# Kernel optimization log

Hardware: AMD Instinct MI355X
Metric: run time of the kernel (lower is better)

The kernel has to match this reference:

```python
import jax, jax.numpy as jnp
import numpy as np

H, DH, CHUNK = 8, 64, 64      # heads, dim_head, chunk_size
DIM = 512
INNER = H * DH                # 512
EPS = 1e-5
SCALE = DH ** -0.5


def _ln(x, g, b):
    m = jnp.mean(x, -1, keepdims=True)
    v = jnp.mean((x - m) ** 2, -1, keepdims=True)
    return (x - m) * jax.lax.rsqrt(v + EPS) * g + b


def _heads(t):
    b, n, _ = t.shape
    return t.reshape(b, n, H, DH).transpose(0, 2, 1, 3)  # b h n d


def _merge(t):
    b, h, n, d = t.shape
    return t.transpose(0, 2, 1, 3).reshape(b, n, h * d)  # b n (h d)


def _local_attn(x, W_qkv, W_ao, b_ao):
    # PreNorm inner Attention: non-overlapping chunked local self-attention
    qkv = x @ W_qkv
    q, k, v = (jnp.split(qkv, 3, axis=-1))
    q, k, v = _heads(q), _heads(k), _heads(v)
    B, Hh, N, D = q.shape
    M = N // CHUNK
    qc = q.reshape(B, Hh, M, CHUNK, D)
    kc = k.reshape(B, Hh, M, CHUNK, D)
    vc = v.reshape(B, Hh, M, CHUNK, D)
    s = jnp.einsum('bhmcd,bhmkd->bhmck', qc, kc) * SCALE
    a = jax.nn.softmax(s, axis=-1)
    o = jnp.einsum('bhmck,bhmkd->bhmcd', a, vc).reshape(B, Hh, N, D)
    return _merge(o) @ W_ao + b_ao


def setup_inputs() -> dict:
    key = jax.random.key(0)
    ks = jax.random.split(key, 10)
    p = lambda k, shp: jax.random.normal(k, shp, dtype=jnp.float32) * 0.02
    return {
        'x':     jax.random.normal(ks[0], (2, 4096, DIM), dtype=jnp.float32),
        'q_x':   jax.random.normal(ks[1], (2, 2048, DIM), dtype=jnp.float32),
        'ln1_g': jnp.ones((DIM,), jnp.float32),
        'ln1_b': jnp.zeros((DIM,), jnp.float32),
        'W_qkv': p(ks[2], (DIM, INNER * 3)),
        'W_ao':  p(ks[3], (INNER, DIM)),
        'b_ao':  jnp.zeros((DIM,), jnp.float32),
        'ln2_g': jnp.ones((DIM,), jnp.float32),
        'ln2_b': jnp.zeros((DIM,), jnp.float32),
        'W_q':   p(ks[4], (DIM, INNER)),
        'W_kv':  p(ks[5], (DIM, INNER * 2)),
        'W_o':   p(ks[6], (INNER, DIM)),
        'b_o':   jnp.zeros((DIM,), jnp.float32),
    }


def reference(x, q_x, ln1_g, ln1_b, W_qkv, W_ao, b_ao,
              ln2_g, ln2_b, W_q, W_kv, W_o, b_o):
    # inner chunked self-attn with PreNorm + residual
    q_in = _local_attn(_ln(q_x, ln1_g, ln1_b), W_qkv, W_ao, b_ao) + q_x
    q_in = _ln(q_in, ln2_g, ln2_b)
    # full cross-attention: queries from q_in, keys/values from x
    q = _heads(q_in @ W_q)
    k, v = jnp.split(x @ W_kv, 2, axis=-1)
    k, v = _heads(k), _heads(v)
    s = jnp.einsum('bhqd,bhkd->bhqk', q, k) * SCALE
    a = jax.nn.softmax(s, axis=-1)
    out = _merge(jnp.einsum('bhqk,bhkd->bhqd', a, v)) @ W_o + b_o
    return (out, q_in)
```

## Files before the change

kernel.cpp:

```cpp
#include <hip/hip_runtime.h>

typedef unsigned short u16;
typedef unsigned int u32;
typedef __attribute__((ext_vector_type(4))) float f32x4;
typedef __attribute__((ext_vector_type(8))) __bf16 bf16x8;

#define NQ 2048
#define NK 4096
#define SCALE 0.125f
#define LOG2E 1.44269504088896f

__device__ __forceinline__ u16 f2bf(float f) {
  u32 x = __float_as_uint(f);
  return (u16)((x + 0x7fffu + ((x >> 16) & 1u)) >> 16);
}

__device__ __forceinline__ float bf2f(u16 b) {
  return __uint_as_float(((u32)b) << 16);
}

__device__ __forceinline__ int swz(int row, int colbyte) {
  return row * 128 + (colbyte ^ ((row & 7) << 4));
}

__device__ __forceinline__ void async16(u16* lds, const u16* g) {
  __builtin_amdgcn_global_load_lds(
      (const __attribute__((address_space(1))) void*)g,
      (__attribute__((address_space(3))) void*)lds, 16, 0, 0);
}

__device__ __forceinline__ f32x4 mfma16(bf16x8 a, bf16x8 b, f32x4 c) {
  return __builtin_amdgcn_mfma_f32_16x16x32_bf16(a, b, c, 0, 0, 0);
}

__device__ __forceinline__ float max16(const f32x4* s) {
  float a = fmaxf(fmaxf(s[0][0], s[0][1]), fmaxf(s[0][2], s[0][3]));
  float b = fmaxf(fmaxf(s[1][0], s[1][1]), fmaxf(s[1][2], s[1][3]));
  float c = fmaxf(fmaxf(s[2][0], s[2][1]), fmaxf(s[2][2], s[2][3]));
  float d = fmaxf(fmaxf(s[3][0], s[3][1]), fmaxf(s[3][2], s[3][3]));
  return fmaxf(fmaxf(a, b), fmaxf(c, d));
}

__global__ __launch_bounds__(256) void k_prep(
    const float* __restrict__ Wqkv, const float* __restrict__ Wao,
    const float* __restrict__ Wq, const float* __restrict__ Wkv,
    const float* __restrict__ Wo, const float* __restrict__ x,
    const float* __restrict__ qx, const float* __restrict__ ln1g,
    const float* __restrict__ ln1b,
    u16* __restrict__ o_qkv, u16* __restrict__ o_ao, u16* __restrict__ o_q,
    u16* __restrict__ o_kv, u16* __restrict__ o_o, u16* __restrict__ x_bf,
    u16* __restrict__ xn_bf) {
  int bid = blockIdx.x;
  int t = threadIdx.x;
  if (bid < 8192) {
    int idx = bid * 256 + t;
    int r = idx >> 9, k = idx & 511;
    const float* in;
    u16* out;
    int N, n;
    if (r < 1536)      { in = Wqkv; out = o_qkv; N = 1536; n = r; }
    else if (r < 2048) { in = Wao;  out = o_ao;  N = 512;  n = r - 1536; }
    else if (r < 2560) { in = Wq;   out = o_q;   N = 512;  n = r - 2048; }
    else if (r < 3584) { in = Wkv;  out = o_kv;  N = 1024; n = r - 2560; }
    else               { in = Wo;   out = o_o;   N = 512;  n = r - 3584; }
    out[(size_t)n * 512 + k] = f2bf(in[(size_t)k * N + n]);
  } else if (bid < 10240) {
    size_t i = ((size_t)(bid - 8192) * 256 + t) * 8;
    float v[8];
    *(float4*)&v[0] = *(const float4*)(x + i);
    *(float4*)&v[4] = *(const float4*)(x + i + 4);
    u16 o[8];
#pragma unroll
    for (int j = 0; j < 8; j++) o[j] = f2bf(v[j]);
    *(uint4*)(x_bf + i) = *(uint4*)o;
  } else {
    int row = (bid - 10240) * 4 + (t >> 6);
    int lane = t & 63;
    size_t base = (size_t)row * 512 + lane * 8;
    float v[8];
    *(float4*)&v[0] = *(const float4*)(qx + base);
    *(float4*)&v[4] = *(const float4*)(qx + base + 4);
    float s = 0.f, q = 0.f;
#pragma unroll
    for (int j = 0; j < 8; j++) { s += v[j]; q += v[j] * v[j]; }
#pragma unroll
    for (int d = 1; d < 64; d <<= 1) {
      s += __shfl_xor(s, d, 64);
      q += __shfl_xor(q, d, 64);
    }
    float mean = s * (1.f / 512.f);
    float var = q * (1.f / 512.f) - mean * mean;
    float rstd = rsqrtf(var + 1e-5f);
    float gv[8], bv[8];
    *(float4*)&gv[0] = *(const float4*)(ln1g + lane * 8);
    *(float4*)&gv[4] = *(const float4*)(ln1g + lane * 8 + 4);
    *(float4*)&bv[0] = *(const float4*)(ln1b + lane * 8);
    *(float4*)&bv[4] = *(const float4*)(ln1b + lane * 8 + 4);
    u16 ob[8];
#pragma unroll
    for (int j = 0; j < 8; j++)
      ob[j] = f2bf((v[j] - mean) * rstd * gv[j] + bv[j]);
    *(uint4*)(xn_bf + base) = *(uint4*)ob;
  }
}

__global__ __launch_bounds__(64) void k_ln(const float* __restrict__ xin,
                                           const float* __restrict__ res,
                                           const float* __restrict__ gg,
                                           const float* __restrict__ bb,
                                           float* __restrict__ fout,
                                           u16* __restrict__ bfout) {
  int row = blockIdx.x, t = threadIdx.x;
  size_t base = (size_t)row * 512 + t * 8;
  float v[8];
  *(float4*)&v[0] = *(const float4*)(xin + base);
  *(float4*)&v[4] = *(const float4*)(xin + base + 4);
  if (res) {
    float r2[8];
    *(float4*)&r2[0] = *(const float4*)(res + base);
    *(float4*)&r2[4] = *(const float4*)(res + base + 4);
#pragma unroll
    for (int j = 0; j < 8; j++) v[j] += r2[j];
  }
  float s = 0.f, q = 0.f;
#pragma unroll
  for (int j = 0; j < 8; j++) { s += v[j]; q += v[j] * v[j]; }
#pragma unroll
  for (int d = 1; d < 64; d <<= 1) {
    s += __shfl_xor(s, d, 64);
    q += __shfl_xor(q, d, 64);
  }
  float mean = s * (1.f / 512.f);
  float var = q * (1.f / 512.f) - mean * mean;
  float rstd = rsqrtf(var + 1e-5f);
  float gv[8], bv[8];
  *(float4*)&gv[0] = *(const float4*)(gg + t * 8);
  *(float4*)&gv[4] = *(const float4*)(gg + t * 8 + 4);
  *(float4*)&bv[0] = *(const float4*)(bb + t * 8);
  *(float4*)&bv[4] = *(const float4*)(bb + t * 8 + 4);
  float y[8];
  u16 ob[8];
#pragma unroll
  for (int j = 0; j < 8; j++) {
    y[j] = (v[j] - mean) * rstd * gv[j] + bv[j];
    ob[j] = f2bf(y[j]);
  }
  if (fout) {
    *(float4*)(fout + base) = *(float4*)&y[0];
    *(float4*)(fout + base + 4) = *(float4*)&y[4];
  }
  if (bfout) *(uint4*)(bfout + base) = *(uint4*)ob;
}

__global__ __launch_bounds__(256) void k_mm0(
    const u16* __restrict__ xb, const u16* __restrict__ wkv,
    const u16* __restrict__ xn, const u16* __restrict__ wqkv,
    u16* __restrict__ kpk, u16* __restrict__ vtp, u16* __restrict__ qkv) {
  __shared__ u16 As[8192];
  __shared__ u16 Bs[8192];
  const int tid = threadIdx.x;
  const int lane = tid & 63, wid = tid >> 6;
  const int lr = lane & 15, g = lane >> 4;
  const int wr = wid >> 1, wc = wid & 1;
  const int srow = wid * 8 + (lane >> 3);
  const int scol = ((lane & 7) ^ (lane >> 3)) << 3;
  u16* lA = As + wid * 512;
  u16* lB = Bs + wid * 512;
  const size_t rK = (size_t)32 * 512;
  int bid = blockIdx.x;
  if (bid < 512) {
    int bx = bid & 7, by = bid >> 3;
    const int rowBase = by * 128, colBase = bx * 128;
    f32x4 acc[4][4] = {};
    const u16* gA = xb + (size_t)(rowBase + srow) * 512 + scol;
    const u16* gB = wkv + (size_t)(colBase + srow) * 512 + scol;
    for (int k0 = 0; k0 < 512; k0 += 64) {
#pragma unroll
      for (int r = 0; r < 4; r++) async16(lA + r * 2048, gA + r * rK + k0);
#pragma unroll
      for (int r = 0; r < 4; r++) async16(lB + r * 2048, gB + r * rK + k0);
      __syncthreads();
#pragma unroll
      for (int kk = 0; kk < 2; kk++) {
        bf16x8 af[4], bw[4];
#pragma unroll
        for (int fm = 0; fm < 4; fm++) {
          int row = wr * 64 + fm * 16 + lr;
          af[fm] = *(const bf16x8*)((const char*)As + row * 128 +
                                    (((kk * 4 + g) ^ (row & 7)) << 4));
        }
#pragma unroll
        for (int fn = 0; fn < 4; fn++) {
          int row = wc * 64 + fn * 16 + lr;
          bw[fn] = *(const bf16x8*)((const char*)Bs + row * 128 +
                                    (((kk * 4 + g) ^ (row & 7)) << 4));
        }
#pragma unroll
        for (int fm = 0; fm < 4; fm++)
#pragma unroll
          for (int fn = 0; fn < 4; fn++)
            acc[fm][fn] = mfma16(af[fm], bw[fn], acc[fm][fn]);
      }
      __syncthreads();
    }
#pragma unroll
    for (int fm = 0; fm < 4; fm++) {
#pragma unroll
      for (int fn = 0; fn < 4; fn++) {
        int row = rowBase + wr * 64 + fm * 16 + g * 4;
        int col = colBase + wc * 64 + fn * 16 + lr;
        int b = row >> 12, n = row & 4095, kt = n >> 6, key0 = n & 63;
        int h = (col >> 6) & 7, d = col & 63;
        size_t tbase = ((size_t)(((b << 3) + h) << 6) + kt) * 4096;
        if (col < 512) {
          u16* kd = kpk + tbase + (size_t)key0 * 64 + d;
          kd[0] = f2bf(acc[fm][fn][0]);
          kd[64] = f2bf(acc[fm][fn][1]);
          kd[128] = f2bf(acc[fm][fn][2]);
          kd[192] = f2bf(acc[fm][fn][3]);
        } else {
          u16 p4[4] = {f2bf(acc[fm][fn][0]), f2bf(acc[fm][fn][1]),
                       f2bf(acc[fm][fn][2]), f2bf(acc[fm][fn][3])};
          *(uint2*)(vtp + tbase + (size_t)d * 64 + key0) = *(uint2*)p4;
        }
      }
    }
  } else {
    int j = bid - 512;
    int bx = j % 12, by = j / 12;
    const int rowBase = by * 64, colBase = bx * 128;
    f32x4 acc[2][4] = {};
    const u16* gA = xn + (size_t)(rowBase + srow) * 512 + scol;
    const u16* gB = wqkv + (size_t)(colBase + srow) * 512 + scol;
    for (int k0 = 0; k0 < 512; k0 += 64) {
#pragma unroll
      for (int r = 0; r < 2; r++) async16(lA + r * 2048, gA + r * rK + k0);
#pragma unroll
      for (int r = 0; r < 4; r++) async16(lB + r * 2048, gB + r * rK + k0);
      __syncthreads();
#pragma unroll
      for (int kk = 0; kk < 2; kk++) {
        bf16x8 af[2], bw[4];
#pragma unroll
        for (int fm = 0; fm < 2; fm++) {
          int row = wr * 32 + fm * 16 + lr;
          af[fm] = *(const bf16x8*)((const char*)As + row * 128 +
                                    (((kk * 4 + g) ^ (row & 7)) << 4));
        }
#pragma unroll
        for (int fn = 0; fn < 4; fn++) {
          int row = wc * 64 + fn * 16 + lr;
          bw[fn] = *(const bf16x8*)((const char*)Bs + row * 128 +
                                    (((kk * 4 + g) ^ (row & 7)) << 4));
        }
#pragma unroll
        for (int fm = 0; fm < 2; fm++)
#pragma unroll
          for (int fn = 0; fn < 4; fn++)
            acc[fm][fn] = mfma16(af[fm], bw[fn], acc[fm][fn]);
      }
      __syncthreads();
    }
#pragma unroll
    for (int fm = 0; fm < 2; fm++) {
#pragma unroll
      for (int fn = 0; fn < 4; fn++) {
        int row = rowBase + wr * 32 + fm * 16 + g * 4;
        int col = colBase + wc * 64 + fn * 16 + lr;
#pragma unroll
        for (int r = 0; r < 4; r++)
          qkv[(size_t)(row + r) * 1536 + col] = f2bf(acc[fm][fn][r]);
      }
    }
  }
}

template <bool BIAS, bool OBF16>
__global__ __launch_bounds__(256) void k_gemm3(const u16* __restrict__ A,
                                               const u16* __restrict__ Bt,
                                               const float* __restrict__ bias,
                                               void* __restrict__ C, int M, int N, int K) {
  __shared__ u16 As[4096];
  __shared__ u16 Bs[4096];
  const int tid = threadIdx.x;
  const int lane = tid & 63, wid = tid >> 6;
  const int lr = lane & 15, g = lane >> 4;
  const int wr = wid >> 1, wc = wid & 1;
  const int rowBase = blockIdx.y * 64, colBase = blockIdx.x * 64;
  f32x4 acc[2][2] = {};
  const int srow = wid * 8 + (lane >> 3);
  const int scol = ((lane & 7) ^ (lane >> 3)) << 3;
  const u16* gA = A + (size_t)(rowBase + srow) * K + scol;
  const u16* gB = Bt + (size_t)(colBase + srow) * K + scol;
  u16* lA = As + wid * 512;
  u16* lB = Bs + wid * 512;
  const size_t rK = (size_t)32 * K;
  for (int k0 = 0; k0 < K; k0 += 64) {
#pragma unroll
    for (int r = 0; r < 2; r++) async16(lA + r * 2048, gA + r * rK + k0);
#pragma unroll
    for (int r = 0; r < 2; r++) async16(lB + r * 2048, gB + r * rK + k0);
    __syncthreads();
#pragma unroll
    for (int kk = 0; kk < 2; kk++) {
      bf16x8 af[2], bw[2];
#pragma unroll
      for (int fm = 0; fm < 2; fm++) {
        int row = wr * 32 + fm * 16 + lr;
        af[fm] = *(const bf16x8*)((const char*)As + row * 128 +
                                  (((kk * 4 + g) ^ (row & 7)) << 4));
      }
#pragma unroll
      for (int fn = 0; fn < 2; fn++) {
        int row = wc * 32 + fn * 16 + lr;
        bw[fn] = *(const bf16x8*)((const char*)Bs + row * 128 +
                                  (((kk * 4 + g) ^ (row & 7)) << 4));
      }
#pragma unroll
      for (int fm = 0; fm < 2; fm++)
#pragma unroll
        for (int fn = 0; fn < 2; fn++)
          acc[fm][fn] = mfma16(af[fm], bw[fn], acc[fm][fn]);
    }
    __syncthreads();
  }
#pragma unroll
  for (int fm = 0; fm < 2; fm++) {
#pragma unroll
    for (int fn = 0; fn < 2; fn++) {
      int row = rowBase + wr * 32 + fm * 16 + g * 4;
      int col = colBase + wc * 32 + fn * 16 + lr;
      float bvv = BIAS ? bias[col] : 0.f;
#pragma unroll
      for (int r = 0; r < 4; r++) {
        float v = acc[fm][fn][r] + bvv;
        if (OBF16)
          ((u16*)C)[(size_t)(row + r) * N + col] = f2bf(v);
        else
          ((float*)C)[(size_t)(row + r) * N + col] = v;
      }
    }
  }
}

__global__ __launch_bounds__(256) void k_local(const u16* __restrict__ qkv,
                                               u16* __restrict__ oattn) {
  int bid = blockIdx.x;
  int m = bid & 31, h = (bid >> 5) & 7, b = bid >> 8;
  __shared__ u16 Qs[4096], Ks[4096], Vt[4096], Ps[4096];
  int t = threadIdx.x;
  {
    int i = t >> 2, c0 = (t & 3) * 16;
    const u16* base = qkv + (size_t)(b * NQ + m * 64 + i) * 1536 + c0;
    uint4 q0 = *(const uint4*)(base + h * 64);
    uint4 q1 = *(const uint4*)(base + h * 64 + 8);
    uint4 k0 = *(const uint4*)(base + 512 + h * 64);
    uint4 k1 = *(const uint4*)(base + 512 + h * 64 + 8);
    uint4 v0 = *(const uint4*)(base + 1024 + h * 64);
    uint4 v1 = *(const uint4*)(base + 1024 + h * 64 + 8);
    *(uint4*)((char*)Qs + swz(i, c0 * 2)) = q0;
    *(uint4*)((char*)Qs + swz(i, c0 * 2 + 16)) = q1;
    *(uint4*)((char*)Ks + swz(i, c0 * 2)) = k0;
    *(uint4*)((char*)Ks + swz(i, c0 * 2 + 16)) = k1;
    u16 vv[16];
    *(uint4*)&vv[0] = v0;
    *(uint4*)&vv[8] = v1;
#pragma unroll
    for (int j = 0; j < 16; j++) {
      int d = c0 + j;
      *(u16*)((char*)Vt + swz(d, i * 2)) = vv[j];
    }
  }
  __syncthreads();
  int lane = t & 63, w = t >> 6, lr = lane & 15, g = lane >> 4;
  bf16x8 aq[2];
#pragma unroll
  for (int kk = 0; kk < 2; kk++)
    aq[kk] = *(const bf16x8*)((const char*)Qs + swz(w * 16 + lr, kk * 64 + g * 16));
  f32x4 s[4] = {};
#pragma unroll
  for (int fn = 0; fn < 4; fn++)
#pragma unroll
    for (int kk = 0; kk < 2; kk++) {
      bf16x8 bk = *(const bf16x8*)((const char*)Ks + swz(fn * 16 + lr, kk * 64 + g * 16));
      s[fn] = mfma16(aq[kk], bk, s[fn]);
    }
  float mx[4], sm[4], p[4][4];
#pragma unroll
  for (int r = 0; r < 4; r++)
    mx[r] = fmaxf(fmaxf(s[0][r], s[1][r]), fmaxf(s[2][r], s[3][r]));
#pragma unroll
  for (int d = 1; d < 16; d <<= 1)
#pragma unroll
    for (int r = 0; r < 4; r++) mx[r] = fmaxf(mx[r], __shfl_xor(mx[r], d, 64));
#pragma unroll
  for (int r = 0; r < 4; r++) {
    float a = 0.f;
#pragma unroll
    for (int fn = 0; fn < 4; fn++) {
      p[fn][r] = exp2f((s[fn][r] - mx[r]) * (SCALE * LOG2E));
      a += p[fn][r];
    }
    sm[r] = a;
  }
#pragma unroll
  for (int d = 1; d < 16; d <<= 1)
#pragma unroll
    for (int r = 0; r < 4; r++) sm[r] += __shfl_xor(sm[r], d, 64);
  float rinv[4];
#pragma unroll
  for (int r = 0; r < 4; r++) rinv[r] = 1.f / sm[r];
#pragma unroll
  for (int fn = 0; fn < 4; fn++)
#pragma unroll
    for (int r = 0; r < 4; r++)
      *(u16*)((char*)Ps + swz(w * 16 + g * 4 + r, (fn * 16 + lr) * 2)) =
          f2bf(p[fn][r] * rinv[r]);
  bf16x8 ap[2];
#pragma unroll
  for (int kk = 0; kk < 2; kk++)
    ap[kk] = *(const bf16x8*)((const char*)Ps + swz(w * 16 + lr, kk * 64 + g * 16));
  f32x4 o[4] = {};
#pragma unroll
  for (int fn = 0; fn < 4; fn++)
#pragma unroll
    for (int kk = 0; kk < 2; kk++) {
      bf16x8 bv = *(const bf16x8*)((const char*)Vt + swz(fn * 16 + lr, kk * 64 + g * 16));
      o[fn] = mfma16(ap[kk], bv, o[fn]);
    }
#pragma unroll
  for (int fn = 0; fn < 4; fn++)
#pragma unroll
    for (int r = 0; r < 4; r++)
      oattn[(size_t)(b * NQ + m * 64 + w * 16 + g * 4 + r) * 512 + h * 64 + fn * 16 + lr] =
          f2bf(o[fn][r]);
}

__global__ __launch_bounds__(256, 4) void k_cross(const u16* __restrict__ q,
                                                  const u16* __restrict__ kpk,
                                                  const u16* __restrict__ vtp,
                                                  u16* __restrict__ opart,
                                                  float* __restrict__ ml) {
  int f = blockIdx.x + 16 * blockIdx.y + 256 * blockIdx.z;
  int xcd = f & 7, j = f >> 3;
  int c = xcd + 8 * (j >> 4);
  int qt = j & 15, bh = c & 15, split = c >> 4;
  int b = bh >> 3, h = bh & 7;
  int t = threadIdx.x, lane = t & 63, w = t >> 6, lr = lane & 15, g = lane >> 4;
  __shared__ u16 Ks[2][4096], Vs[2][4096];
  const float cs = SCALE * LOG2E;

  bf16x8 ones;
#pragma unroll
  for (int i = 0; i < 8; i++) ones[i] = (__bf16)1.0f;

  int srow = w * 16 + (lane >> 3);
  int scolb = ((lane & 7) ^ (srow & 7)) << 3;
  int kperm = ((srow >> 5) << 5) + (((srow >> 2) & 3) << 3) +
              (((srow >> 4) & 1) << 2) + (srow & 3);
  int ksoff0 = kperm * 64 + scolb;
  int ksoff1 = ksoff0 + 1024;
  int soff0 = srow * 64 + scolb;
  int soff1 = soff0 + 512;
  const u16* ktiles = kpk + ((size_t)(bh * 64 + split * 16) * 4096);
  const u16* vtiles = vtp + ((size_t)(bh * 64 + split * 16) * 4096);

  const u16* qrowL = q + (size_t)(b * NQ + qt * 128 + w * 32 + lr) * 512 + h * 64;
  const u16* qrowH = qrowL + 16 * 512;
  bf16x8 aqL0 = *(const bf16x8*)(qrowL + g * 8);
  bf16x8 aqL1 = *(const bf16x8*)(qrowL + 32 + g * 8);
  bf16x8 aqH0 = *(const bf16x8*)(qrowH + g * 8);
  bf16x8 aqH1 = *(const bf16x8*)(qrowH + 32 + g * 8);

  f32x4 oL[4] = {}, oH[4] = {};
  f32x4 lsumL = {}, lsumH = {};
  float mL = -1e30f, mH = -1e30f;

  async16(&Ks[0][w * 1024], ktiles + ksoff0);
  async16(&Ks[0][w * 1024 + 512], ktiles + ksoff1);
  async16(&Vs[0][w * 1024], vtiles + soff0);
  async16(&Vs[0][w * 1024 + 512], vtiles + soff1);
  __syncthreads();

  int buf = 0;
  for (int kt = 0; kt < 16; kt++) {
    if (kt < 15) {
      const u16* kn = ktiles + (size_t)(kt + 1) * 4096;
      const u16* vn = vtiles + (size_t)(kt + 1) * 4096;
      async16(&Ks[buf ^ 1][w * 1024], kn + ksoff0);
      async16(&Ks[buf ^ 1][w * 1024 + 512], kn + ksoff1);
      async16(&Vs[buf ^ 1][w * 1024], vn + soff0);
      async16(&Vs[buf ^ 1][w * 1024 + 512], vn + soff1);
    }
    f32x4 stL[4], stH[4];
    __builtin_amdgcn_s_setprio(1);
#pragma unroll
    for (int fm = 0; fm < 4; fm++) {
      bf16x8 bk0 = *(const bf16x8*)((const char*)Ks[buf] + swz(fm * 16 + lr, g * 16));
      bf16x8 bk1 = *(const bf16x8*)((const char*)Ks[buf] + swz(fm * 16 + lr, 64 + g * 16));
      stL[fm] = mfma16(bk0, aqL0, (f32x4){0.f, 0.f, 0.f, 0.f});
      stL[fm] = mfma16(bk1, aqL1, stL[fm]);
      stH[fm] = mfma16(bk0, aqH0, (f32x4){0.f, 0.f, 0.f, 0.f});
      stH[fm] = mfma16(bk1, aqH1, stH[fm]);
    }
    __builtin_amdgcn_s_setprio(0);
    float tmL = max16(stL);
    tmL = fmaxf(tmL, __shfl_xor(tmL, 16, 64));
    tmL = fmaxf(tmL, __shfl_xor(tmL, 32, 64));
    if (!__all(tmL <= mL + 22.2f)) {
      float mnew = fmaxf(mL, tmL);
      float corr = exp2f((mL - mnew) * cs);
      mL = mnew;
      float c0 = __shfl(corr, g * 4 + 0, 64);
      float c1 = __shfl(corr, g * 4 + 1, 64);
      float c2 = __shfl(corr, g * 4 + 2, 64);
      float c3 = __shfl(corr, g * 4 + 3, 64);
      lsumL[0] *= c0; lsumL[1] *= c1; lsumL[2] *= c2; lsumL[3] *= c3;
#pragma unroll
      for (int fn = 0; fn < 4; fn++) {
        oL[fn][0] *= c0; oL[fn][1] *= c1; oL[fn][2] *= c2; oL[fn][3] *= c3;
      }
    }
    bf16x8 apL0, apL1;
    {
      float mc = mL * cs;
      union { __bf16 hh[8]; bf16x8 v; } u0, u1;
#pragma unroll
      for (int r = 0; r < 4; r++) {
        u0.hh[r]     = (__bf16)exp2f(stL[0][r] * cs - mc);
        u0.hh[4 + r] = (__bf16)exp2f(stL[1][r] * cs - mc);
        u1.hh[r]     = (__bf16)exp2f(stL[2][r] * cs - mc);
        u1.hh[4 + r] = (__bf16)exp2f(stL[3][r] * cs - mc);
      }
      apL0 = u0.v;
      apL1 = u1.v;
    }
    float tmH = max16(stH);
    tmH = fmaxf(tmH, __shfl_xor(tmH, 16, 64));
    tmH = fmaxf(tmH, __shfl_xor(tmH, 32, 64));
    if (!__all(tmH <= mH + 22.2f)) {
      float mnew = fmaxf(mH, tmH);
      float corr = exp2f((mH - mnew) * cs);
      mH = mnew;
      float c0 = __shfl(corr, g * 4 + 0, 64);
      float c1 = __shfl(corr, g * 4 + 1, 64);
      float c2 = __shfl(corr, g * 4 + 2, 64);
      float c3 = __shfl(corr, g * 4 + 3, 64);
      lsumH[0] *= c0; lsumH[1] *= c1; lsumH[2] *= c2; lsumH[3] *= c3;
#pragma unroll
      for (int fn = 0; fn < 4; fn++) {
        oH[fn][0] *= c0; oH[fn][1] *= c1; oH[fn][2] *= c2; oH[fn][3] *= c3;
      }
    }
    bf16x8 apH0, apH1;
    {
      float mc = mH * cs;
      union { __bf16 hh[8]; bf16x8 v; } u0, u1;
#pragma unroll
      for (int r = 0; r < 4; r++) {
        u0.hh[r]     = (__bf16)exp2f(stH[0][r] * cs - mc);
        u0.hh[4 + r] = (__bf16)exp2f(stH[1][r] * cs - mc);
        u1.hh[r]     = (__bf16)exp2f(stH[2][r] * cs - mc);
        u1.hh[4 + r] = (__bf16)exp2f(stH[3][r] * cs - mc);
      }
      apH0 = u0.v;
      apH1 = u1.v;
    }
    __builtin_amdgcn_s_setprio(1);
    lsumL = mfma16(apL0, ones, lsumL);
    lsumL = mfma16(apL1, ones, lsumL);
    lsumH = mfma16(apH0, ones, lsumH);
    lsumH = mfma16(apH1, ones, lsumH);
#pragma unroll
    for (int fn = 0; fn < 4; fn++) {
      bf16x8 bv0 = *(const bf16x8*)((const char*)Vs[buf] + swz(fn * 16 + lr, g * 16));
      bf16x8 bv1 = *(const bf16x8*)((const char*)Vs[buf] + swz(fn * 16 + lr, 64 + g * 16));
      oL[fn] = mfma16(apL0, bv0, oL[fn]);
      oL[fn] = mfma16(apL1, bv1, oL[fn]);
      oH[fn] = mfma16(apH0, bv0, oH[fn]);
      oH[fn] = mfma16(apH1, bv1, oH[fn]);
    }
    __builtin_amdgcn_s_setprio(0);
    __syncthreads();
    buf ^= 1;
  }
  size_t sb = ((size_t)(split * 16 + bh) * NQ) + qt * 128 + w * 32;
  {
    float r0 = 1.f / lsumL[0], r1 = 1.f / lsumL[1];
    float r2 = 1.f / lsumL[2], r3 = 1.f / lsumL[3];
#pragma unroll
    for (int fn = 0; fn < 4; fn++) {
      opart[(sb + g * 4 + 0) * 64 + fn * 16 + lr] = f2bf(oL[fn][0] * r0);
      opart[(sb + g * 4 + 1) * 64 + fn * 16 + lr] = f2bf(oL[fn][1] * r1);
      opart[(sb + g * 4 + 2) * 64 + fn * 16 + lr] = f2bf(oL[fn][2] * r2);
      opart[(sb + g * 4 + 3) * 64 + fn * 16 + lr] = f2bf(oL[fn][3] * r3);
    }
  }
  {
    float r0 = 1.f / lsumH[0], r1 = 1.f / lsumH[1];
    float r2 = 1.f / lsumH[2], r3 = 1.f / lsumH[3];
#pragma unroll
    for (int fn = 0; fn < 4; fn++) {
      opart[(sb + 16 + g * 4 + 0) * 64 + fn * 16 + lr] = f2bf(oH[fn][0] * r0);
      opart[(sb + 16 + g * 4 + 1) * 64 + fn * 16 + lr] = f2bf(oH[fn][1] * r1);
      opart[(sb + 16 + g * 4 + 2) * 64 + fn * 16 + lr] = f2bf(oH[fn][2] * r2);
      opart[(sb + 16 + g * 4 + 3) * 64 + fn * 16 + lr] = f2bf(oH[fn][3] * r3);
    }
  }
  if (g == 0) {
    ml[(sb + lr) * 2] = mL;
    ml[(sb + 16 + lr) * 2] = mH;
  }
  if (lr == 0) {
#pragma unroll
    for (int r = 0; r < 4; r++) {
      ml[(sb + g * 4 + r) * 2 + 1] = lsumL[r];
      ml[(sb + 16 + g * 4 + r) * 2 + 1] = lsumH[r];
    }
  }
}

__global__ __launch_bounds__(256) void k_comb(const u16* __restrict__ opart,
                                              const float* __restrict__ ml,
                                              u16* __restrict__ co) {
  int idx = blockIdx.x * 256 + threadIdx.x;
  int c8 = idx & 7;
  int row = (idx >> 3) & 2047;
  int bh = idx >> 14;
  int b = bh >> 3, h = bh & 7;
  const float cs = SCALE * LOG2E;
  float m[4], l[4];
#pragma unroll
  for (int s = 0; s < 4; s++) {
    size_t rb = ((size_t)(s * 16 + bh) * NQ + row);
    m[s] = ml[rb * 2];
    l[s] = ml[rb * 2 + 1];
  }
  float M = fmaxf(fmaxf(m[0], m[1]), fmaxf(m[2], m[3]));
  float wsum = 0.f, wgt[4];
#pragma unroll
  for (int s = 0; s < 4; s++) {
    wgt[s] = l[s] * exp2f((m[s] - M) * cs);
    wsum += wgt[s];
  }
  float acc[8] = {};
#pragma unroll
  for (int s = 0; s < 4; s++) {
    size_t rb = ((size_t)(s * 16 + bh) * NQ + row);
    uint4 pk = *(const uint4*)(opart + rb * 64 + c8 * 8);
    u16 pe[8];
    *(uint4*)pe = pk;
#pragma unroll
    for (int j = 0; j < 8; j++) acc[j] += wgt[s] * bf2f(pe[j]);
  }
  float rw = 1.f / wsum;
  u16 ob[8];
#pragma unroll
  for (int j = 0; j < 8; j++) ob[j] = f2bf(acc[j] * rw);
  *(uint4*)(co + ((size_t)(b * NQ + row) * 512) + h * 64 + c8 * 8) = *(uint4*)ob;
}

extern "C" void kernel_launch(void* const* d_in, const int* in_sizes, int n_in,
                              void* d_out, int out_size, void* d_ws, size_t ws_size,
                              hipStream_t stream) {
  const float* x    = (const float*)d_in[0];
  const float* qx   = (const float*)d_in[1];
  const float* ln1g = (const float*)d_in[2];
  const float* ln1b = (const float*)d_in[3];
  const float* Wqkv = (const float*)d_in[4];
  const float* Wao  = (const float*)d_in[5];
  const float* bao  = (const float*)d_in[6];
  const float* ln2g = (const float*)d_in[7];
  const float* ln2b = (const float*)d_in[8];
  const float* Wq   = (const float*)d_in[9];
  const float* Wkv  = (const float*)d_in[10];
  const float* Wo   = (const float*)d_in[11];
  const float* bo   = (const float*)d_in[12];
  float* out_p = (float*)d_out;
  float* qin_p = out_p + (size_t)2 * 2048 * 512;

  const size_t MiB = 1048576;
  char* ws = (char*)d_ws;
  u16* w_qkv_t = (u16*)(ws);
  u16* w_ao_t  = (u16*)(ws + 1572864);
  u16* w_q_t   = (u16*)(ws + 2097152);
  u16* w_kv_t  = (u16*)(ws + 2621440);
  u16* w_o_t   = (u16*)(ws + 3670016);
  u16* kpk     = (u16*)(ws + 4 * MiB);
  u16* vtp     = (u16*)(ws + 12 * MiB);
  u16* x_bf    = (u16*)(ws + 20 * MiB);
  u16* oattn_bf = (u16*)(ws + 20 * MiB);
  float* ao_f  = (float*)(ws + 24 * MiB);
  u16* xn_bf   = (u16*)(ws + 28 * MiB);
  u16* qin_bf  = (u16*)(ws + 32 * MiB);
  u16* opart   = (u16*)(ws + 20 * MiB);
  u16* qkv_bf  = (u16*)(ws + 36 * MiB);
  u16* q_bf    = (u16*)(ws + 36 * MiB);
  u16* co_bf   = (u16*)(ws + 40 * MiB);
  float* ml    = out_p;

  k_prep<<<dim3(8192 + 2048 + 1024), 256, 0, stream>>>(
      Wqkv, Wao, Wq, Wkv, Wo, x, qx, ln1g, ln1b,
      w_qkv_t, w_ao_t, w_q_t, w_kv_t, w_o_t, x_bf, xn_bf);
  k_mm0<<<dim3(512 + 768), 256, 0, stream>>>(
      x_bf, w_kv_t, xn_bf, w_qkv_t, kpk, vtp, qkv_bf);
  k_local<<<dim3(512), 256, 0, stream>>>(qkv_bf, oattn_bf);
  k_gemm3<true, false><<<dim3(512 / 64, 4096 / 64), 256, 0, stream>>>(
      oattn_bf, w_ao_t, bao, ao_f, 4096, 512, 512);
  k_ln<<<dim3(4096), 64, 0, stream>>>(ao_f, qx, ln2g, ln2b, qin_p, qin_bf);
  k_gemm3<false, true><<<dim3(512 / 64, 4096 / 64), 256, 0, stream>>>(
      qin_bf, w_q_t, nullptr, q_bf, 4096, 512, 512);
  k_cross<<<dim3(16, 16, 4), 256, 0, stream>>>(q_bf, kpk, vtp, opart, ml);
  k_comb<<<dim3(262144 / 256), 256, 0, stream>>>(opart, ml, co_bf);
  k_gemm3<true, false><<<dim3(512 / 64, 4096 / 64), 256, 0, stream>>>(
      co_bf, w_o_t, bo, out_p, 4096, 512, 512);
}
```

Baseline: 153.8 us.

## Fuse split-KV combine into output projection GEMM and store ao in bf16

```diff
diff --git a/kernel.cpp b/kernel.cpp
--- a/kernel.cpp
+++ b/kernel.cpp
@@ -104,7 +104,7 @@
   }
 }
 
-__global__ __launch_bounds__(64) void k_ln(const float* __restrict__ xin,
+__global__ __launch_bounds__(64) void k_ln(const u16* __restrict__ xin,
                                            const float* __restrict__ res,
                                            const float* __restrict__ gg,
                                            const float* __restrict__ bb,
@@ -112,10 +112,12 @@
                                            u16* __restrict__ bfout) {
   int row = blockIdx.x, t = threadIdx.x;
   size_t base = (size_t)row * 512 + t * 8;
+  u16 xv[8];
+  *(uint4*)xv = *(const uint4*)(xin + base);
   float v[8];
-  *(float4*)&v[0] = *(const float4*)(xin + base);
-  *(float4*)&v[4] = *(const float4*)(xin + base + 4);
-  if (res) {
+#pragma unroll
+  for (int j = 0; j < 8; j++) v[j] = bf2f(xv[j]);
+  {
     float r2[8];
     *(float4*)&r2[0] = *(const float4*)(res + base);
     *(float4*)&r2[4] = *(const float4*)(res + base + 4);
@@ -145,11 +147,9 @@
     y[j] = (v[j] - mean) * rstd * gv[j] + bv[j];
     ob[j] = f2bf(y[j]);
   }
-  if (fout) {
-    *(float4*)(fout + base) = *(float4*)&y[0];
-    *(float4*)(fout + base + 4) = *(float4*)&y[4];
-  }
-  if (bfout) *(uint4*)(bfout + base) = *(uint4*)ob;
+  *(float4*)(fout + base) = *(float4*)&y[0];
+  *(float4*)(fout + base + 4) = *(float4*)&y[4];
+  *(uint4*)(bfout + base) = *(uint4*)ob;
 }
 
 __global__ __launch_bounds__(256) void k_mm0(
@@ -343,6 +343,105 @@
   }
 }
 
+__global__ __launch_bounds__(256) void k_gout(const u16* __restrict__ opart,
+                                              const float* __restrict__ ml,
+                                              const u16* __restrict__ wo_t,
+                                              const float* __restrict__ bias,
+                                              float* __restrict__ C) {
+  __shared__ u16 As[4096];
+  __shared__ u16 Bs[4096];
+  const int tid = threadIdx.x;
+  const int lane = tid & 63, wid = tid >> 6;
+  const int lr = lane & 15, g = lane >> 4;
+  const int wr = wid >> 1, wc = wid & 1;
+  const int rowBase = blockIdx.y * 64, colBase = blockIdx.x * 64;
+  f32x4 acc[2][2] = {};
+  const int srow = wid * 8 + (lane >> 3);
+  const int slot = lane & 7;
+  const int scolB = ((lane & 7) ^ (lane >> 3)) << 3;
+  const u16* gB = wo_t + (size_t)(colBase + srow) * 512 + scolB;
+  u16* lB = Bs + wid * 512;
+  const size_t rK = (size_t)32 * 512;
+  const float cs = SCALE * LOG2E;
+  for (int k0 = 0; k0 < 512; k0 += 64) {
+#pragma unroll
+    for (int r = 0; r < 2; r++) async16(lB + r * 2048, gB + r * rK + k0);
+    int h = k0 >> 6;
+#pragma unroll
+    for (int r = 0; r < 2; r++) {
+      int lrow = srow + r * 32;
+      int row = rowBase + lrow;
+      int b = row >> 11, nq = row & 2047;
+      int bh = (b << 3) + h;
+      size_t rr[4];
+      float mm[4], ll[4];
+#pragma unroll
+      for (int s = 0; s < 4; s++) {
+        rr[s] = ((size_t)(s * 16 + bh) * 2048 + nq);
+        mm[s] = ml[rr[s] * 2];
+        ll[s] = ml[rr[s] * 2 + 1];
+      }
+      float M = fmaxf(fmaxf(mm[0], mm[1]), fmaxf(mm[2], mm[3]));
+      float wn[4], wsum = 0.f;
+#pragma unroll
+      for (int s = 0; s < 4; s++) {
+        wn[s] = ll[s] * exp2f((mm[s] - M) * cs);
+        wsum += wn[s];
+      }
+      float rw = 1.f / wsum;
+#pragma unroll
+      for (int s = 0; s < 4; s++) wn[s] *= rw;
+      float a8[8] = {};
+#pragma unroll
+      for (int s = 0; s < 4; s++) {
+        u16 pe[8];
+        *(uint4*)pe = *(const uint4*)(opart + rr[s] * 64 + slot * 8);
+#pragma unroll
+        for (int j = 0; j < 8; j++) a8[j] += wn[s] * bf2f(pe[j]);
+      }
+      u16 o8[8];
+#pragma unroll
+      for (int j = 0; j < 8; j++) o8[j] = f2bf(a8[j]);
+      *(uint4*)((char*)As + lrow * 128 + ((slot ^ (lrow & 7)) << 4)) = *(uint4*)o8;
+    }
+    __syncthreads();
+#pragma unroll
+    for (int kk = 0; kk < 2; kk++) {
+      bf16x8 af[2], bw[2];
+#pragma unroll
+      for (int fm = 0; fm < 2; fm++) {
+        int row = wr * 32 + fm * 16 + lr;
+        af[fm] = *(const bf16x8*)((const char*)As + row * 128 +
+                                  (((kk * 4 + g) ^ (row & 7)) << 4));
+      }
+#pragma unroll
+      for (int fn = 0; fn < 2; fn++) {
+        int row = wc * 32 + fn * 16 + lr;
+        bw[fn] = *(const bf16x8*)((const char*)Bs + row * 128 +
+                                  (((kk * 4 + g) ^ (row & 7)) << 4));
+      }
+#pragma unroll
+      for (int fm = 0; fm < 2; fm++)
+#pragma unroll
+        for (int fn = 0; fn < 2; fn++)
+          acc[fm][fn] = mfma16(af[fm], bw[fn], acc[fm][fn]);
+    }
+    __syncthreads();
+  }
+#pragma unroll
+  for (int fm = 0; fm < 2; fm++) {
+#pragma unroll
+    for (int fn = 0; fn < 2; fn++) {
+      int row = rowBase + wr * 32 + fm * 16 + g * 4;
+      int col = colBase + wc * 32 + fn * 16 + lr;
+      float bvv = bias[col];
+#pragma unroll
+      for (int r = 0; r < 4; r++)
+        C[(size_t)(row + r) * 512 + col] = acc[fm][fn][r] + bvv;
+    }
+  }
+}
+
 __global__ __launch_bounds__(256) void k_local(const u16* __restrict__ qkv,
                                                u16* __restrict__ oattn) {
   int bid = blockIdx.x;
@@ -620,46 +719,6 @@
   }
 }
 
-__global__ __launch_bounds__(256) void k_comb(const u16* __restrict__ opart,
-                                              const float* __restrict__ ml,
-                                              u16* __restrict__ co) {
-  int idx = blockIdx.x * 256 + threadIdx.x;
-  int c8 = idx & 7;
-  int row = (idx >> 3) & 2047;
-  int bh = idx >> 14;
-  int b = bh >> 3, h = bh & 7;
-  const float cs = SCALE * LOG2E;
-  float m[4], l[4];
-#pragma unroll
-  for (int s = 0; s < 4; s++) {
-    size_t rb = ((size_t)(s * 16 + bh) * NQ + row);
-    m[s] = ml[rb * 2];
-    l[s] = ml[rb * 2 + 1];
-  }
-  float M = fmaxf(fmaxf(m[0], m[1]), fmaxf(m[2], m[3]));
-  float wsum = 0.f, wgt[4];
-#pragma unroll
-  for (int s = 0; s < 4; s++) {
-    wgt[s] = l[s] * exp2f((m[s] - M) * cs);
-    wsum += wgt[s];
-  }
-  float acc[8] = {};
-#pragma unroll
-  for (int s = 0; s < 4; s++) {
-    size_t rb = ((size_t)(s * 16 + bh) * NQ + row);
-    uint4 pk = *(const uint4*)(opart + rb * 64 + c8 * 8);
-    u16 pe[8];
-    *(uint4*)pe = pk;
-#pragma unroll
-    for (int j = 0; j < 8; j++) acc[j] += wgt[s] * bf2f(pe[j]);
-  }
-  float rw = 1.f / wsum;
-  u16 ob[8];
-#pragma unroll
-  for (int j = 0; j < 8; j++) ob[j] = f2bf(acc[j] * rw);
-  *(uint4*)(co + ((size_t)(b * NQ + row) * 512) + h * 64 + c8 * 8) = *(uint4*)ob;
-}
-
 extern "C" void kernel_launch(void* const* d_in, const int* in_sizes, int n_in,
                               void* d_out, int out_size, void* d_ws, size_t ws_size,
                               hipStream_t stream) {
@@ -686,18 +745,17 @@
   u16* w_q_t   = (u16*)(ws + 2097152);
   u16* w_kv_t  = (u16*)(ws + 2621440);
   u16* w_o_t   = (u16*)(ws + 3670016);
+  float* ml    = (float*)(ws);
   u16* kpk     = (u16*)(ws + 4 * MiB);
   u16* vtp     = (u16*)(ws + 12 * MiB);
   u16* x_bf    = (u16*)(ws + 20 * MiB);
   u16* oattn_bf = (u16*)(ws + 20 * MiB);
-  float* ao_f  = (float*)(ws + 24 * MiB);
+  u16* ao_bf   = (u16*)(ws + 24 * MiB);
   u16* xn_bf   = (u16*)(ws + 28 * MiB);
   u16* qin_bf  = (u16*)(ws + 32 * MiB);
   u16* opart   = (u16*)(ws + 20 * MiB);
   u16* qkv_bf  = (u16*)(ws + 36 * MiB);
   u16* q_bf    = (u16*)(ws + 36 * MiB);
-  u16* co_bf   = (u16*)(ws + 40 * MiB);
-  float* ml    = out_p;
 
   k_prep<<<dim3(8192 + 2048 + 1024), 256, 0, stream>>>(
       Wqkv, Wao, Wq, Wkv, Wo, x, qx, ln1g, ln1b,
@@ -705,13 +763,12 @@
   k_mm0<<<dim3(512 + 768), 256, 0, stream>>>(
       x_bf, w_kv_t, xn_bf, w_qkv_t, kpk, vtp, qkv_bf);
   k_local<<<dim3(512), 256, 0, stream>>>(qkv_bf, oattn_bf);
-  k_gemm3<true, false><<<dim3(512 / 64, 4096 / 64), 256, 0, stream>>>(
-      oattn_bf, w_ao_t, bao, ao_f, 4096, 512, 512);
-  k_ln<<<dim3(4096), 64, 0, stream>>>(ao_f, qx, ln2g, ln2b, qin_p, qin_bf);
+  k_gemm3<true, true><<<dim3(512 / 64, 4096 / 64), 256, 0, stream>>>(
+      oattn_bf, w_ao_t, bao, ao_bf, 4096, 512, 512);
+  k_ln<<<dim3(4096), 64, 0, stream>>>(ao_bf, qx, ln2g, ln2b, qin_p, qin_bf);
   k_gemm3<false, true><<<dim3(512 / 64, 4096 / 64), 256, 0, stream>>>(
       qin_bf, w_q_t, nullptr, q_bf, 4096, 512, 512);
   k_cross<<<dim3(16, 16, 4), 256, 0, stream>>>(q_bf, kpk, vtp, opart, ml);
-  k_comb<<<dim3(262144 / 256), 256, 0, stream>>>(opart, ml, co_bf);
-  k_gemm3<true, false><<<dim3(512 / 64, 4096 / 64), 256, 0, stream>>>(
-      co_bf, w_o_t, bo, out_p, 4096, 512, 512);
-}
+  k_gout<<<dim3(512 / 64, 4096 / 64), 256, 0, stream>>>(
+      opart, ml, w_o_t, bo, out_p);
+}
```

Result: slower. 177.6 us (+15.5%).
